# Optimization experiments

Measured on AMD Instinct MI355X. Metric: run time of the kernel, lower is better.

The kernel has to match this reference:

```python
import jax, jax.numpy as jnp
import numpy as np

NUM_CLASSES = 2
TOP_K = 1500
CONF_THRESH = 0.01
NMS_THRESH = 0.2
VAR0, VAR1 = 0.1, 0.2  # cfg['variance']


def setup_inputs() -> dict:
    key = jax.random.key(0)
    k1, k2, k3 = jax.random.split(key, 3)
    B, P = 32, 76800
    loc_data = jax.random.normal(k1, (B, P, 4), jnp.float32)
    conf_data = jax.random.uniform(k2, (B * P, NUM_CLASSES), jnp.float32)
    prior_data = jax.random.uniform(k3, (P, 4), jnp.float32)
    return {"loc_data": loc_data, "conf_data": conf_data, "prior_data": prior_data}


def _decode(loc, priors):
    # loc, priors: [P,4]; SSD box decode with variances
    cxcy = priors[:, :2] + loc[:, :2] * VAR0 * priors[:, 2:]
    wh = priors[:, 2:] * jnp.exp(loc[:, 2:] * VAR1)
    x1y1 = cxcy - wh * 0.5
    return jnp.concatenate([x1y1, x1y1 + wh], axis=-1)  # [P,4] (x1,y1,x2,y2)


def _nms_per_class(scores, boxes):
    # scores: [P], boxes: [P,4] -> [TOP_K,5] packed (score,x1,y1,x2,y2)
    s = jnp.where(scores > CONF_THRESH, scores, -jnp.inf)
    sk, idx = jax.lax.top_k(s, TOP_K)  # torch nms keeps only top_k candidates
    bk = boxes[idx]
    x1, y1, x2, y2 = bk[:, 0], bk[:, 1], bk[:, 2], bk[:, 3]
    area = (x2 - x1) * (y2 - y1)
    iota = jnp.arange(TOP_K)

    def step(active, i):
        # greedy NMS over score-descending candidates
        xx1 = jnp.maximum(x1, x1[i]); yy1 = jnp.maximum(y1, y1[i])
        xx2 = jnp.minimum(x2, x2[i]); yy2 = jnp.minimum(y2, y2[i])
        inter = jnp.maximum(xx2 - xx1, 0.0) * jnp.maximum(yy2 - yy1, 0.0)
        iou = inter / (area + area[i] - inter)
        kept = active[i]
        suppress = (iou > NMS_THRESH) & (iota != i)
        active = jnp.where(kept, active & ~suppress, active)
        return active, kept

    _, keep = jax.lax.scan(step, sk > -jnp.inf, iota)
    rows = jnp.where(keep[:, None], jnp.concatenate([sk[:, None], bk], axis=1), 0.0)
    # pack kept rows at the front (score-descending order), zeros after
    rank = jnp.cumsum(keep) - 1
    dest = jnp.where(keep, rank, TOP_K)  # dump non-kept into scratch slot
    return jnp.zeros((TOP_K + 1, 5), bk.dtype).at[dest].set(rows)[:TOP_K]


def reference(loc_data, conf_data, prior_data):
    B, P, _ = loc_data.shape
    conf = conf_data.reshape(B, P, NUM_CLASSES)
    decoded = jax.vmap(_decode, in_axes=(0, None))(loc_data, prior_data)  # [B,P,4]
    outs = []
    for cl in range(1, NUM_CLASSES):  # background class 0 stays zero
        outs.append(jax.vmap(_nms_per_class)(conf[:, :, cl], decoded))
    bg = jnp.zeros((B, 1, TOP_K, 5), decoded.dtype)
    return jnp.concatenate([bg, jnp.stack(outs, axis=1)], axis=1)  # [B,C,TOP_K,5]
```

## Files before the change

### kernel.cpp

```cpp
#include <hip/hip_runtime.h>
#include <stdint.h>

typedef unsigned long long u64;
typedef unsigned int u32;

#define NUM_B 32
#define NUM_P 76800
#define TOPK 1500
#define NBINS 4096
#define CAP 2048
#define NWORDS 24
#define NCHUNK 6
#define CPAD 32
#define HSLICES 16
#define HCHUNK (NUM_P / HSLICES)

__device__ __forceinline__ u32 fbits(float f) { return __float_as_uint(f); }
__device__ __forceinline__ int binOf(float s) {
    int b = (int)(s * (float)NBINS);
    return (b > NBINS - 1) ? NBINS - 1 : b;
}
__device__ __forceinline__ u64 readlane64(u64 v, int l) {
    u32 lo = (u32)__builtin_amdgcn_readlane((int)(u32)(v & 0xffffffffu), l);
    u32 hi = (u32)__builtin_amdgcn_readlane((int)(u32)(v >> 32), l);
    return ((u64)hi << 32) | lo;
}

__global__ __launch_bounds__(256) void hist_kernel(const float4* __restrict__ conf4,
                                                   u32* __restrict__ hist,
                                                   u32* __restrict__ counts) {
    int c = blockIdx.x, b = blockIdx.y, tid = threadIdx.x;
    if (c == 0 && tid < CPAD) counts[(size_t)b * CPAD + tid] = 0;
    __shared__ u32 h[NBINS];
    for (int i = tid; i < NBINS; i += 256) h[i] = 0;
    __syncthreads();
    const float4* base = conf4 + (size_t)b * (NUM_P / 2) + (size_t)c * (HCHUNK / 2);
    for (int i = tid; i < HCHUNK / 2; i += 256) {
        float4 v = base[i];
        if (v.y > 0.01f) atomicAdd(&h[binOf(v.y)], 1u);
        if (v.w > 0.01f) atomicAdd(&h[binOf(v.w)], 1u);
    }
    __syncthreads();
    u32* outp = hist + ((size_t)b * HSLICES + c) * NBINS;
    for (int i = tid; i < NBINS; i += 256) outp[i] = h[i];
}

__global__ void thresh_kernel(const u32* __restrict__ hist, int* __restrict__ tbin) {
    int b = blockIdx.x;
    int tid = threadIdx.x;
    const u32* hb = hist + (size_t)b * HSLICES * NBINS;
    __shared__ u32 vals[256];
    __shared__ int s_min;
    u32 total = 0;
    for (int c = 0; c < NBINS / 256; ++c) {
        if (tid == 0) s_min = 256;
        int bin = NBINS - 1 - (c * 256 + tid);
        u32 v = 0;
#pragma unroll
        for (int s = 0; s < HSLICES; ++s) v += hb[(size_t)s * NBINS + bin];
        __syncthreads();
        vals[tid] = v;
        __syncthreads();
        for (int off = 1; off < 256; off <<= 1) {
            u32 add = (tid >= off) ? vals[tid - off] : 0;
            __syncthreads();
            vals[tid] += add;
            __syncthreads();
        }
        u32 cum = total + vals[tid];
        if (cum >= TOPK) atomicMin(&s_min, tid);
        __syncthreads();
        if (s_min < 256) {
            if (tid == 0) tbin[b] = NBINS - 1 - (c * 256 + s_min);
            return;
        }
        total += vals[255];
    }
    if (tid == 0) tbin[b] = 0;
}

__global__ __launch_bounds__(256) void compact_kernel(
    const float4* __restrict__ conf4, const int* __restrict__ tbin,
    u32* __restrict__ counts, u64* __restrict__ keys) {
    int b = blockIdx.y;
    int tid = threadIdx.x;
    int lane = tid & 63, wave = tid >> 6;
    int f4 = blockIdx.x * 256 + tid;
    float4 c = conf4[(size_t)b * (NUM_P / 2) + f4];
    int tb = tbin[b];
    int p0 = f4 * 2, p1 = p0 + 1;
    bool v0 = (c.y > 0.01f) && (binOf(c.y) >= tb);
    bool v1 = (c.w > 0.01f) && (binOf(c.w) >= tb);

    u64 m0 = __ballot(v0), m1 = __ballot(v1);
    u32 c0 = (u32)__popcll(m0);
    u64 below = (1ULL << lane) - 1ULL;
    u32 off0 = (u32)__popcll(m0 & below);
    u32 off1 = c0 + (u32)__popcll(m1 & below);
    u32 wtot = c0 + (u32)__popcll(m1);

    __shared__ u32 wcnt[4];
    __shared__ u32 s_base;
    if (lane == 0) wcnt[wave] = wtot;
    __syncthreads();
    if (tid == 0) {
        u32 tot = wcnt[0] + wcnt[1] + wcnt[2] + wcnt[3];
        s_base = (tot > 0) ? atomicAdd(&counts[(size_t)b * CPAD], tot) : 0u;
    }
    __syncthreads();
    u32 woff = 0;
    for (int w = 0; w < wave; ++w) woff += wcnt[w];
    if (v0) {
        u32 pos = s_base + woff + off0;
        if (pos < CAP) keys[(size_t)b * CAP + pos] = ((u64)fbits(c.y) << 32) | (u32)(~p0);
    }
    if (v1) {
        u32 pos = s_base + woff + off1;
        if (pos < CAP) keys[(size_t)b * CAP + pos] = ((u64)fbits(c.w) << 32) | (u32)(~p1);
    }
}

__global__ __launch_bounds__(256) void rank_decode_kernel(
    const u64* __restrict__ keys, const u32* __restrict__ counts,
    const float* __restrict__ loc, const float* __restrict__ prior,
    float* __restrict__ sscore, float* __restrict__ sbox) {
#pragma clang fp contract(off)
    int blk = blockIdx.x, b = blockIdx.y, tid = threadIdx.x;
    __shared__ u64 k[CAP];
    int n = (int)min(counts[(size_t)b * CPAD], (u32)CAP);
    for (int t = tid; t < CAP; t += 256)
        k[t] = (t < n) ? keys[(size_t)b * CAP + t] : 0ULL;
    __syncthreads();

    int t = blk * 256 + tid;
    u64 mykey = k[t];
    if (mykey == 0ULL) return;

    u32 rank = 0;
#pragma unroll 8
    for (int j = 0; j < CAP; ++j) rank += (k[j] > mykey) ? 1u : 0u;

    if (rank < TOPK) {
        u32 pidx = ~(u32)mykey;
        float sc = __uint_as_float((u32)(mykey >> 32));
        const float* lp = &loc[((size_t)b * NUM_P + pidx) * 4];
        const float* pp = &prior[(size_t)pidx * 4];
        float lx = lp[0], ly = lp[1], lw = lp[2], lh = lp[3];
        float pcx = pp[0], pcy = pp[1], pw = pp[2], ph = pp[3];
        float cx = pcx + (lx * 0.1f) * pw;
        float cy = pcy + (ly * 0.1f) * ph;
        float w  = pw * expf(lw * 0.2f);
        float h  = ph * expf(lh * 0.2f);
        float x1 = cx - w * 0.5f;
        float y1 = cy - h * 0.5f;
        float x2 = x1 + w;
        float y2 = y1 + h;
        sscore[(size_t)b * TOPK + rank] = sc;
        float* bx = &sbox[((size_t)b * TOPK + rank) * 4];
        bx[0] = x1; bx[1] = y1; bx[2] = x2; bx[3] = y2;
    }
}

__global__ __launch_bounds__(256) void mask_kernel(
    const float* __restrict__ sbox, u64* __restrict__ mask) {
#pragma clang fp contract(off)
    int w = blockIdx.x, c = blockIdx.y, b = blockIdx.z, tid = threadIdx.x;
    int i = c * 256 + tid;
    if ((w * 64 + 63) <= (c * 256)) return;
    __shared__ float4 cbox[64];
    __shared__ float car[64];
    if (tid < 64) {
        int j = w * 64 + tid;
        float4 bx = make_float4(0.f, 0.f, 0.f, 0.f);
        if (j < TOPK) bx = ((const float4*)sbox)[(size_t)b * TOPK + j];
        cbox[tid] = bx;
        car[tid] = (bx.z - bx.x) * (bx.w - bx.y);
    }
    __syncthreads();
    if (i < TOPK && (w * 64 + 63) > i) {
        const double MID = 0.5 * ((double)__uint_as_float(0x3E4CCCCDu) +
                                  (double)__uint_as_float(0x3E4CCCCEu));
        const float4 bx = ((const float4*)sbox)[(size_t)b * TOPK + i];
        float x1i = bx.x, y1i = bx.y, x2i = bx.z, y2i = bx.w;
        float ai = (x2i - x1i) * (y2i - y1i);
        u64 jmask = (i < w * 64) ? ~0ULL : (~0ULL << (i - w * 64 + 1));
        u64 m = 0;
        for (int j2 = 0; j2 < 64; ++j2) {
            float4 cb = cbox[j2];
            float xx1 = fmaxf(cb.x, x1i);
            float yy1 = fmaxf(cb.y, y1i);
            float xx2 = fminf(cb.z, x2i);
            float yy2 = fminf(cb.w, y2i);
            float iw = fmaxf(xx2 - xx1, 0.0f);
            float ih = fmaxf(yy2 - yy1, 0.0f);
            float inter = iw * ih;
            float denom = (car[j2] + ai) - inter;
            if ((double)inter >= MID * (double)denom) m |= (1ULL << j2);
        }
        m &= jmask;
        mask[((size_t)b * NWORDS + w) * TOPK + i] = m;
    }
}

__global__ __launch_bounds__(256) void sweep_kernel(
    const u64* __restrict__ mask, const float* __restrict__ sscore,
    const float* __restrict__ sbox, float* __restrict__ out) {
    int b = blockIdx.x, tid = threadIdx.x;
    int lane = tid & 63, wid = tid >> 6;

    const u64* mbase = mask + (size_t)b * NWORDS * TOPK;

    __shared__ u64 rowbuf[3][NWORDS][65];
    __shared__ u64 aw[NWORDS];
    __shared__ u32 pfx[NWORDS + 1];

    u64 act = 0;
    u64 sv[8];
    if (wid == 0) {
        for (int c = 0; c < NWORDS; ++c) {
            int r = c * 64 + lane;
            bool v = (r < TOPK) && (sscore[(size_t)b * TOPK + r] > 0.0f);
            u64 m = __ballot(v);
            if (lane == c) act = m;
        }
    } else {
        int w0 = (wid - 1) * 8;
#pragma unroll
        for (int t = 0; t < 2; ++t) {
            u64 tmp[8];
#pragma unroll
            for (int k = 0; k < 8; ++k)
                tmp[k] = (w0 + k >= t) ? mbase[(size_t)(w0 + k) * TOPK + t * 64 + lane] : 0ULL;
#pragma unroll
            for (int k = 0; k < 8; ++k)
                rowbuf[t][w0 + k][lane] = tmp[k];
        }
        {
            int rr = 2 * 64 + lane;
#pragma unroll
            for (int k = 0; k < 8; ++k)
                sv[k] = (w0 + k >= 2) ? mbase[(size_t)(w0 + k) * TOPK + rr] : 0ULL;
        }
    }
    __syncthreads();

    for (int T = 0; T < NWORDS; ++T) {
        if (wid == 0) {
            u64 dreg = rowbuf[T % 3][T][lane];
            u64 actw = readlane64(act, T);
            u64 kept = 0, rem = actw;
            while (rem) {
                int i2 = __ffsll(rem) - 1;
                kept |= (1ULL << i2);
                rem &= rem - 1;
                rem &= ~readlane64(dreg, i2);
            }
            if (lane == T) act = kept;
            if (lane > T && lane < NWORDS) {
                u64 kb = kept;
                while (kb) {
                    int r = __ffsll(kb) - 1;
                    kb &= kb - 1;
                    act &= ~rowbuf[T % 3][lane][r];
                }
            }
        } else {
            int tw = T + 2;
            if (tw < NWORDS) {
                int w0 = (wid - 1) * 8;
#pragma unroll
                for (int k = 0; k < 8; ++k)
                    rowbuf[tw % 3][w0 + k][lane] = sv[k];
                int tn = T + 3;
                if (tn < NWORDS) {
                    int rr = tn * 64 + lane;
                    bool vr = rr < TOPK;
#pragma unroll
                    for (int k = 0; k < 8; ++k)
                        sv[k] = (vr && (w0 + k >= tn))
                                    ? mbase[(size_t)(w0 + k) * TOPK + rr] : 0ULL;
                }
            }
        }
        __syncthreads();
    }

    if (wid == 0 && lane < NWORDS) aw[lane] = act;
    {
        float* p0 = out + ((size_t)b * 2 + 0) * TOPK * 5;
        float* p1 = out + ((size_t)b * 2 + 1) * TOPK * 5;
        for (int t = tid; t < TOPK * 5; t += 256) { p0[t] = 0.0f; p1[t] = 0.0f; }
    }
    __syncthreads();
    if (tid == 0) {
        u32 acc = 0;
        for (int wd = 0; wd < NWORDS; ++wd) { pfx[wd] = acc; acc += (u32)__popcll(aw[wd]); }
        pfx[NWORDS] = acc;
    }
    __syncthreads();
    for (int r = tid; r < TOPK; r += 256) {
        int wd = r >> 6;
        u64 word = aw[wd];
        if ((word >> (r & 63)) & 1ULL) {
            u32 rank = pfx[wd] + (u32)__popcll(word & ((1ULL << (r & 63)) - 1ULL));
            float sc = sscore[(size_t)b * TOPK + r];
            float4 bx = ((const float4*)sbox)[(size_t)b * TOPK + r];
            size_t base_o = (((size_t)b * 2 + 1) * TOPK + (size_t)rank) * 5;
            out[base_o + 0] = sc;
            out[base_o + 1] = bx.x;
            out[base_o + 2] = bx.y;
            out[base_o + 3] = bx.z;
            out[base_o + 4] = bx.w;
        }
    }
}

extern "C" void kernel_launch(void* const* d_in, const int* in_sizes, int n_in,
                              void* d_out, int out_size, void* d_ws, size_t ws_size,
                              hipStream_t stream) {
    const float* loc   = (const float*)d_in[0];
    const float* conf  = (const float*)d_in[1];
    const float* prior = (const float*)d_in[2];
    float* out = (float*)d_out;
    char* ws = (char*)d_ws;

    u64* mask_buf = (u64*)(ws + 0);
    u32* hist     = (u32*)(ws + 0);
    u64* keys     = (u64*)(ws + 8388608);
    u32* counts   = (u32*)(ws + 8912896);
    int* tbin     = (int*)(ws + 8916992);
    float* sscore = (float*)(ws + 9216000);
    float* sbox   = (float*)(ws + 9408000);

    hist_kernel<<<dim3(HSLICES, 32), 256, 0, stream>>>((const float4*)conf, hist, counts);
    thresh_kernel<<<32, 256, 0, stream>>>(hist, tbin);
    compact_kernel<<<dim3(150, 32), 256, 0, stream>>>((const float4*)conf, tbin, counts, keys);
    rank_decode_kernel<<<dim3(CAP / 256, 32), 256, 0, stream>>>(keys, counts, loc, prior,
                                                                sscore, sbox);
    mask_kernel<<<dim3(NWORDS, NCHUNK, 32), 256, 0, stream>>>(sbox, mask_buf);
    sweep_kernel<<<32, 256, 0, stream>>>(mask_buf, sscore, sbox, out);
}
```

Baseline: 193.4 us.

## Bucket-sort compacted candidates by histogram bin to shrink rank computation

The threshold kernel now records each bin's exclusive prefix offset and count. The compaction kernel scatters candidates into per-bin slots with per-bin atomics, so keys end up grouped by descending bin. Ranking then only compares a key against the other keys in its own bin instead of all 2048 slots. The histogram shrinks to 2048 bins and output zeroing uses float4 stores. This adds more contended global atomics in compaction, and bins become wider, so ranking work depends on how many keys share a bin.

```diff
diff --git a/kernel.cpp b/kernel.cpp
--- a/kernel.cpp
+++ b/kernel.cpp
@@ -7,11 +7,10 @@
 #define NUM_B 32
 #define NUM_P 76800
 #define TOPK 1500
-#define NBINS 4096
+#define NBINS 2048
 #define CAP 2048
 #define NWORDS 24
 #define NCHUNK 6
-#define CPAD 32
 #define HSLICES 16
 #define HCHUNK (NUM_P / HSLICES)
 
@@ -28,9 +27,9 @@
 
 __global__ __launch_bounds__(256) void hist_kernel(const float4* __restrict__ conf4,
                                                    u32* __restrict__ hist,
-                                                   u32* __restrict__ counts) {
+                                                   u32* __restrict__ bpos) {
     int c = blockIdx.x, b = blockIdx.y, tid = threadIdx.x;
-    if (c == 0 && tid < CPAD) counts[(size_t)b * CPAD + tid] = 0;
+    if (tid < NBINS / HSLICES) bpos[(size_t)b * NBINS + c * (NBINS / HSLICES) + tid] = 0;
     __shared__ u32 h[NBINS];
     for (int i = tid; i < NBINS; i += 256) h[i] = 0;
     __syncthreads();
@@ -45,7 +44,9 @@
     for (int i = tid; i < NBINS; i += 256) outp[i] = h[i];
 }
 
-__global__ void thresh_kernel(const u32* __restrict__ hist, int* __restrict__ tbin) {
+__global__ void thresh_kernel(const u32* __restrict__ hist, int* __restrict__ tbin,
+                              u32* __restrict__ binbase, u32* __restrict__ bincnt,
+                              u32* __restrict__ ntotal) {
     int b = blockIdx.x;
     int tid = threadIdx.x;
     const u32* hb = hist + (size_t)b * HSLICES * NBINS;
@@ -68,81 +69,70 @@
             __syncthreads();
         }
         u32 cum = total + vals[tid];
+        binbase[(size_t)b * NBINS + bin] = cum - v;
+        bincnt [(size_t)b * NBINS + bin] = v;
         if (cum >= TOPK) atomicMin(&s_min, tid);
         __syncthreads();
         if (s_min < 256) {
-            if (tid == 0) tbin[b] = NBINS - 1 - (c * 256 + s_min);
+            if (tid == 0) {
+                tbin[b] = NBINS - 1 - (c * 256 + s_min);
+                ntotal[b] = total + vals[s_min];
+            }
             return;
         }
         total += vals[255];
     }
-    if (tid == 0) tbin[b] = 0;
+    if (tid == 0) { tbin[b] = 0; ntotal[b] = total; }
 }
 
 __global__ __launch_bounds__(256) void compact_kernel(
     const float4* __restrict__ conf4, const int* __restrict__ tbin,
-    u32* __restrict__ counts, u64* __restrict__ keys) {
+    const u32* __restrict__ binbase, u32* __restrict__ bpos,
+    u64* __restrict__ keys) {
     int b = blockIdx.y;
     int tid = threadIdx.x;
-    int lane = tid & 63, wave = tid >> 6;
     int f4 = blockIdx.x * 256 + tid;
     float4 c = conf4[(size_t)b * (NUM_P / 2) + f4];
     int tb = tbin[b];
     int p0 = f4 * 2, p1 = p0 + 1;
-    bool v0 = (c.y > 0.01f) && (binOf(c.y) >= tb);
-    bool v1 = (c.w > 0.01f) && (binOf(c.w) >= tb);
-
-    u64 m0 = __ballot(v0), m1 = __ballot(v1);
-    u32 c0 = (u32)__popcll(m0);
-    u64 below = (1ULL << lane) - 1ULL;
-    u32 off0 = (u32)__popcll(m0 & below);
-    u32 off1 = c0 + (u32)__popcll(m1 & below);
-    u32 wtot = c0 + (u32)__popcll(m1);
-
-    __shared__ u32 wcnt[4];
-    __shared__ u32 s_base;
-    if (lane == 0) wcnt[wave] = wtot;
-    __syncthreads();
-    if (tid == 0) {
-        u32 tot = wcnt[0] + wcnt[1] + wcnt[2] + wcnt[3];
-        s_base = (tot > 0) ? atomicAdd(&counts[(size_t)b * CPAD], tot) : 0u;
-    }
-    __syncthreads();
-    u32 woff = 0;
-    for (int w = 0; w < wave; ++w) woff += wcnt[w];
-    if (v0) {
-        u32 pos = s_base + woff + off0;
+
+    int b0 = binOf(c.y);
+    if (c.y > 0.01f && b0 >= tb) {
+        u32 slot = atomicAdd(&bpos[(size_t)b * NBINS + b0], 1u);
+        u32 pos = binbase[(size_t)b * NBINS + b0] + slot;
         if (pos < CAP) keys[(size_t)b * CAP + pos] = ((u64)fbits(c.y) << 32) | (u32)(~p0);
     }
-    if (v1) {
-        u32 pos = s_base + woff + off1;
+    int b1 = binOf(c.w);
+    if (c.w > 0.01f && b1 >= tb) {
+        u32 slot = atomicAdd(&bpos[(size_t)b * NBINS + b1], 1u);
+        u32 pos = binbase[(size_t)b * NBINS + b1] + slot;
         if (pos < CAP) keys[(size_t)b * CAP + pos] = ((u64)fbits(c.w) << 32) | (u32)(~p1);
     }
 }
 
 __global__ __launch_bounds__(256) void rank_decode_kernel(
-    const u64* __restrict__ keys, const u32* __restrict__ counts,
+    const u64* __restrict__ keys, const u32* __restrict__ binbase,
+    const u32* __restrict__ bincnt, const u32* __restrict__ ntotal,
     const float* __restrict__ loc, const float* __restrict__ prior,
     float* __restrict__ sscore, float* __restrict__ sbox) {
 #pragma clang fp contract(off)
-    int blk = blockIdx.x, b = blockIdx.y, tid = threadIdx.x;
-    __shared__ u64 k[CAP];
-    int n = (int)min(counts[(size_t)b * CPAD], (u32)CAP);
-    for (int t = tid; t < CAP; t += 256)
-        k[t] = (t < n) ? keys[(size_t)b * CAP + t] : 0ULL;
-    __syncthreads();
-
-    int t = blk * 256 + tid;
-    u64 mykey = k[t];
-    if (mykey == 0ULL) return;
-
-    u32 rank = 0;
-#pragma unroll 8
-    for (int j = 0; j < CAP; ++j) rank += (k[j] > mykey) ? 1u : 0u;
+    int b = blockIdx.y;
+    int g = blockIdx.x * 256 + threadIdx.x;
+    int n = (int)min(ntotal[b], (u32)CAP);
+    if (g >= n) return;
+    const u64* kb = keys + (size_t)b * CAP;
+    u64 mykey = kb[g];
+    float sc = __uint_as_float((u32)(mykey >> 32));
+    int bn = binOf(sc);
+    u32 start = binbase[(size_t)b * NBINS + bn];
+    u32 end = start + bincnt[(size_t)b * NBINS + bn];
+    if (end > (u32)n) end = (u32)n;
+    u32 rank = start;
+#pragma unroll 4
+    for (u32 j = start; j < end; ++j) rank += (kb[j] > mykey) ? 1u : 0u;
 
     if (rank < TOPK) {
         u32 pidx = ~(u32)mykey;
-        float sc = __uint_as_float((u32)(mykey >> 32));
         const float* lp = &loc[((size_t)b * NUM_P + pidx) * 4];
         const float* pp = &prior[(size_t)pidx * 4];
         float lx = lp[0], ly = lp[1], lw = lp[2], lh = lp[3];
@@ -287,9 +277,9 @@
 
     if (wid == 0 && lane < NWORDS) aw[lane] = act;
     {
-        float* p0 = out + ((size_t)b * 2 + 0) * TOPK * 5;
-        float* p1 = out + ((size_t)b * 2 + 1) * TOPK * 5;
-        for (int t = tid; t < TOPK * 5; t += 256) { p0[t] = 0.0f; p1[t] = 0.0f; }
+        float4* pz = (float4*)(out + (size_t)b * 2 * TOPK * 5);
+        float4 z4 = make_float4(0.f, 0.f, 0.f, 0.f);
+        for (int t = tid; t < (2 * TOPK * 5) / 4; t += 256) pz[t] = z4;
     }
     __syncthreads();
     if (tid == 0) {
@@ -326,16 +316,21 @@
 
     u64* mask_buf = (u64*)(ws + 0);
     u32* hist     = (u32*)(ws + 0);
-    u64* keys     = (u64*)(ws + 8388608);
-    u32* counts   = (u32*)(ws + 8912896);
-    int* tbin     = (int*)(ws + 8916992);
+    u32* binbase  = (u32*)(ws + 4194304);
+    u32* bincnt   = (u32*)(ws + 4456448);
+    u32* bpos     = (u32*)(ws + 4718592);
+    u64* keys     = (u64*)(ws + 4980736);
+    int* tbin     = (int*)(ws + 5505024);
+    u32* ntotal   = (u32*)(ws + 5505152);
     float* sscore = (float*)(ws + 9216000);
     float* sbox   = (float*)(ws + 9408000);
 
-    hist_kernel<<<dim3(HSLICES, 32), 256, 0, stream>>>((const float4*)conf, hist, counts);
-    thresh_kernel<<<32, 256, 0, stream>>>(hist, tbin);
-    compact_kernel<<<dim3(150, 32), 256, 0, stream>>>((const float4*)conf, tbin, counts, keys);
-    rank_decode_kernel<<<dim3(CAP / 256, 32), 256, 0, stream>>>(keys, counts, loc, prior,
+    hist_kernel<<<dim3(HSLICES, 32), 256, 0, stream>>>((const float4*)conf, hist, bpos);
+    thresh_kernel<<<32, 256, 0, stream>>>(hist, tbin, binbase, bincnt, ntotal);
+    compact_kernel<<<dim3(150, 32), 256, 0, stream>>>((const float4*)conf, tbin, binbase,
+                                                      bpos, keys);
+    rank_decode_kernel<<<dim3(CAP / 256, 32), 256, 0, stream>>>(keys, binbase, bincnt,
+                                                                ntotal, loc, prior,
                                                                 sscore, sbox);
     mask_kernel<<<dim3(NWORDS, NCHUNK, 32), 256, 0, stream>>>(sbox, mask_buf);
     sweep_kernel<<<32, 256, 0, stream>>>(mask_buf, sscore, sbox, out);
```

New measurement: 178.5 us. 7.7% less time.
